# Kernel tuning notes

Hardware: AMD Instinct MI355X
Metric: run time of the kernel (lower is better)

## Reference

```python
import jax, jax.numpy as jnp
import numpy as np

UNITS = [100, 80, 50, 30]
D_IN = 64


def _lstm_layer(x, Wx, Wh, b):
    # x: [B, T, D]; Wx: [D, 4u]; Wh: [u, 4u]; b: [4u]
    B = x.shape[0]
    u = Wh.shape[0]
    # precompute input contribution for all timesteps: [B, T, 4u]
    xg = jnp.einsum('btd,dg->btg', x, Wx) + b

    def step(carry, xg_t):
        h, c = carry
        g = xg_t + h @ Wh                      # [B, 4u]
        i, f, cbar, o = jnp.split(g, 4, axis=-1)
        i = jax.nn.sigmoid(i)
        f = jax.nn.sigmoid(f)
        o = jax.nn.sigmoid(o)
        c = f * c + i * jnp.tanh(cbar)
        h = o * jnp.tanh(c)
        return (h, c), h

    init = (jnp.zeros((B, u), x.dtype), jnp.zeros((B, u), x.dtype))
    (h_final, _), hs = jax.lax.scan(step, init, jnp.swapaxes(xg, 0, 1))
    return jnp.swapaxes(hs, 0, 1), h_final  # [B, T, u], [B, u]


def setup_inputs() -> dict:
    key = jax.random.key(0)
    ks = jax.random.split(key, 16)
    B, T = 256, 1024
    inp = {"sequence": jax.random.normal(ks[0], (B, T, D_IN), dtype=jnp.float32)}
    d_in = D_IN
    for li, u in enumerate(UNITS):
        s_x = 1.0 / np.sqrt(d_in)
        s_h = 1.0 / np.sqrt(u)
        inp[f"Wx{li}"] = jax.random.normal(ks[1 + 3 * li], (d_in, 4 * u), dtype=jnp.float32) * s_x
        inp[f"Wh{li}"] = jax.random.normal(ks[2 + 3 * li], (u, 4 * u), dtype=jnp.float32) * s_h
        inp[f"b{li}"] = jnp.zeros((4 * u,), dtype=jnp.float32)
        d_in = u
    inp["W_out"] = jax.random.normal(ks[13], (UNITS[-1], 1), dtype=jnp.float32) / np.sqrt(UNITS[-1])
    inp["b_out"] = jnp.zeros((1,), dtype=jnp.float32)
    return inp


def reference(sequence, Wx0, Wh0, b0, Wx1, Wh1, b1, Wx2, Wh2, b2, Wx3, Wh3, b3, W_out, b_out):
    # 4 stacked LSTM layers; dropout is identity at inference.
    x, _ = _lstm_layer(sequence, Wx0, Wh0, b0)   # [B, T, 100]
    x, _ = _lstm_layer(x, Wx1, Wh1, b1)          # [B, T, 80]
    x, _ = _lstm_layer(x, Wx2, Wh2, b2)          # [B, T, 50]
    _, h = _lstm_layer(x, Wx3, Wh3, b3)          # final state [B, 30]
    return h @ W_out + b_out                     # [B, 1]
```

## Files before the change

### kernel.cpp

```cpp
#include <hip/hip_runtime.h>


#define BATCH 256
#define TSTEPS 1024

__device__ __forceinline__ float sigm(float x) {
    return 1.0f / (1.0f + __expf(-x));
}

__device__ __forceinline__ float tanh_fast(float x) {
    float ax = fabsf(x);
    float e = __expf(2.0f * ax);
    float r = 1.0f - 2.0f / (e + 1.0f);
    return copysignf(r, x);
}

template<int DIN, int U, int SPLIT, int S, int BLOCK, bool LAST>
__global__ __launch_bounds__(BLOCK, 1)
void lstm_layer(const float* __restrict__ xin,
                const float* __restrict__ Wx,
                const float* __restrict__ Wh,
                const float* __restrict__ bias,
                float* __restrict__ xout,
                const float* __restrict__ Wout,
                const float* __restrict__ bout,
                float* __restrict__ dout)
{
    constexpr int G  = 4 * U;
    constexpr int K  = DIN + U;
    constexpr int KP = SPLIT * S;
    static_assert(KP >= K, "slice coverage");
    static_assert((S % 4) == 0, "float4 alignment");

    const int b   = blockIdx.x;
    const int tid = threadIdx.x;
    const int u   = tid / SPLIT;
    const int s   = tid % SPLIT;
    const bool active = (u < U);
    const int uu  = active ? u : 0;

    __shared__ __align__(16) float s_xh[2][KP];

    for (int i = tid; i < 2 * KP; i += BLOCK) ((float*)s_xh)[i] = 0.0f;

    float w[4][S];
    float bj[4];
#pragma unroll
    for (int g = 0; g < 4; ++g) {
        const int col = g * U + uu;
        bj[g] = bias[col];
#pragma unroll
        for (int kk = 0; kk < S; ++kk) {
            const int k = s * S + kk;
            float v = 0.0f;
            if (k < DIN)    v = Wx[k * G + col];
            else if (k < K) v = Wh[(k - DIN) * G + col];
            w[g][kk] = v;
        }
    }

    const float* xrow = xin + (size_t)b * TSTEPS * DIN;
    if (tid < DIN) s_xh[0][tid] = xrow[tid];
    __syncthreads();

    float c = 0.0f;
    int cur = 0;

    for (int t = 0; t < TSTEPS; ++t, cur ^= 1) {
        float xn = 0.0f;
        if (t + 1 < TSTEPS && tid < DIN) xn = xrow[(size_t)(t + 1) * DIN + tid];

        float a0 = 0.0f, a1 = 0.0f, a2 = 0.0f, a3 = 0.0f;
        const float* xh = &s_xh[cur][s * S];
#pragma unroll
        for (int kk = 0; kk < S; kk += 4) {
            float4 v = *(const float4*)(xh + kk);
            a0 = fmaf(v.x, w[0][kk + 0], a0);
            a0 = fmaf(v.y, w[0][kk + 1], a0);
            a0 = fmaf(v.z, w[0][kk + 2], a0);
            a0 = fmaf(v.w, w[0][kk + 3], a0);
            a1 = fmaf(v.x, w[1][kk + 0], a1);
            a1 = fmaf(v.y, w[1][kk + 1], a1);
            a1 = fmaf(v.z, w[1][kk + 2], a1);
            a1 = fmaf(v.w, w[1][kk + 3], a1);
            a2 = fmaf(v.x, w[2][kk + 0], a2);
            a2 = fmaf(v.y, w[2][kk + 1], a2);
            a2 = fmaf(v.z, w[2][kk + 2], a2);
            a2 = fmaf(v.w, w[2][kk + 3], a2);
            a3 = fmaf(v.x, w[3][kk + 0], a3);
            a3 = fmaf(v.y, w[3][kk + 1], a3);
            a3 = fmaf(v.z, w[3][kk + 2], a3);
            a3 = fmaf(v.w, w[3][kk + 3], a3);
        }

#pragma unroll
        for (int d = SPLIT >> 1; d > 0; d >>= 1) {
            a0 += __shfl_down(a0, d);
            a1 += __shfl_down(a1, d);
            a2 += __shfl_down(a2, d);
            a3 += __shfl_down(a3, d);
        }

        const int nxt = cur ^ 1;
        if (active && s == 0) {
            const float fi = sigm(a0 + bj[0]);
            const float ff = sigm(a1 + bj[1]);
            const float tc = tanh_fast(a2 + bj[2]);
            const float fo = sigm(a3 + bj[3]);
            c = ff * c + fi * tc;
            const float h = fo * tanh_fast(c);
            s_xh[nxt][DIN + u] = h;
            if (!LAST) xout[((size_t)b * TSTEPS + t) * U + u] = h;
        }
        if (tid < DIN) s_xh[nxt][tid] = xn;
        __syncthreads();
    }

    if (LAST && tid == 0) {
        float acc = bout[0];
#pragma unroll
        for (int k = 0; k < U; ++k) acc = fmaf(s_xh[cur][DIN + k], Wout[k], acc);
        dout[b] = acc;
    }
}

extern "C" void kernel_launch(void* const* d_in, const int* in_sizes, int n_in,
                              void* d_out, int out_size, void* d_ws, size_t ws_size,
                              hipStream_t stream)
{
    const float* seq  = (const float*)d_in[0];
    const float* Wx0  = (const float*)d_in[1];
    const float* Wh0  = (const float*)d_in[2];
    const float* b0   = (const float*)d_in[3];
    const float* Wx1  = (const float*)d_in[4];
    const float* Wh1  = (const float*)d_in[5];
    const float* b1   = (const float*)d_in[6];
    const float* Wx2  = (const float*)d_in[7];
    const float* Wh2  = (const float*)d_in[8];
    const float* b2   = (const float*)d_in[9];
    const float* Wx3  = (const float*)d_in[10];
    const float* Wh3  = (const float*)d_in[11];
    const float* b3   = (const float*)d_in[12];
    const float* Wout = (const float*)d_in[13];
    const float* bout = (const float*)d_in[14];
    float* out = (float*)d_out;

    float* ws = (float*)d_ws;
    float* X1 = ws;
    float* X2 = ws + (size_t)BATCH * TSTEPS * 100;
    float* X3 = ws;

    dim3 grid(BATCH);

    lstm_layer<64, 100, 4, 44, 448, false><<<grid, 448, 0, stream>>>(
        seq, Wx0, Wh0, b0, X1, nullptr, nullptr, nullptr);
    lstm_layer<100, 80, 4, 48, 320, false><<<grid, 320, 0, stream>>>(
        X1, Wx1, Wh1, b1, X2, nullptr, nullptr, nullptr);
    lstm_layer<80, 50, 4, 36, 256, false><<<grid, 256, 0, stream>>>(
        X2, Wx2, Wh2, b2, X3, nullptr, nullptr, nullptr);
    lstm_layer<50, 30, 4, 20, 128, true><<<grid, 128, 0, stream>>>(
        X3, Wx3, Wh3, b3, nullptr, Wout, bout, out);
}
```

Baseline: 3.586 ms.

## Split K across 8 lanes with packed FMA and DPP reduction

Each hidden unit's dot product is now split across 8 threads instead of 4, so blocks are twice as large and each thread holds a shorter weight slice. The inner loop uses two-wide float vectors so the compiler can emit packed FMA instructions, and the cross-lane sum uses DPP row operations in place of shuffle-down. The aim is to shorten the serial per-timestep critical path of the recurrence. In exchange the block is larger, so the per-step barrier covers more waves, and the DPP reduction assumes each group of 8 lanes is aligned inside a row.

```diff
diff --git a/kernel.cpp b/kernel.cpp
--- a/kernel.cpp
+++ b/kernel.cpp
@@ -3,6 +3,29 @@
 
 #define BATCH 256
 #define TSTEPS 1024
+
+typedef float v2f __attribute__((ext_vector_type(2)));
+
+__device__ __forceinline__ v2f fma2(v2f a, v2f b, v2f c) {
+#if __has_builtin(__builtin_elementwise_fma)
+    return __builtin_elementwise_fma(a, b, c);
+#else
+    v2f r; r.x = fmaf(a.x, b.x, c.x); r.y = fmaf(a.y, b.y, c.y); return r;
+#endif
+}
+
+template<int CTRL>
+__device__ __forceinline__ float red_step(float v) {
+    int t = __builtin_amdgcn_update_dpp(0, __float_as_int(v), CTRL, 0xF, 0xF, true);
+    return v + __int_as_float(t);
+}
+
+__device__ __forceinline__ float red8(float v) {
+    v = red_step<0xB1>(v);
+    v = red_step<0x4E>(v);
+    v = red_step<0x141>(v);
+    return v;
+}
 
 __device__ __forceinline__ float sigm(float x) {
     return 1.0f / (1.0f + __expf(-x));
@@ -15,7 +38,7 @@
     return copysignf(r, x);
 }
 
-template<int DIN, int U, int SPLIT, int S, int BLOCK, bool LAST>
+template<int DIN, int U, int S, int BLOCK, bool LAST>
 __global__ __launch_bounds__(BLOCK, 1)
 void lstm_layer(const float* __restrict__ xin,
                 const float* __restrict__ Wx,
@@ -28,14 +51,14 @@
 {
     constexpr int G  = 4 * U;
     constexpr int K  = DIN + U;
-    constexpr int KP = SPLIT * S;
+    constexpr int KP = 8 * S;
     static_assert(KP >= K, "slice coverage");
     static_assert((S % 4) == 0, "float4 alignment");
 
     const int b   = blockIdx.x;
     const int tid = threadIdx.x;
-    const int u   = tid / SPLIT;
-    const int s   = tid % SPLIT;
+    const int u   = tid >> 3;
+    const int s   = tid & 7;
     const bool active = (u < U);
     const int uu  = active ? u : 0;
 
@@ -43,19 +66,24 @@
 
     for (int i = tid; i < 2 * KP; i += BLOCK) ((float*)s_xh)[i] = 0.0f;
 
-    float w[4][S];
+    v2f w2[4][S / 2];
     float bj[4];
 #pragma unroll
     for (int g = 0; g < 4; ++g) {
         const int col = g * U + uu;
         bj[g] = bias[col];
 #pragma unroll
-        for (int kk = 0; kk < S; ++kk) {
-            const int k = s * S + kk;
-            float v = 0.0f;
-            if (k < DIN)    v = Wx[k * G + col];
-            else if (k < K) v = Wh[(k - DIN) * G + col];
-            w[g][kk] = v;
+        for (int j = 0; j < S / 2; ++j) {
+            v2f v;
+#pragma unroll
+            for (int e = 0; e < 2; ++e) {
+                const int k = s * S + 2 * j + e;
+                float x = 0.0f;
+                if (k < DIN)    x = Wx[k * G + col];
+                else if (k < K) x = Wh[(k - DIN) * G + col];
+                v[e] = x;
+            }
+            w2[g][j] = v;
         }
     }
 
@@ -70,43 +98,35 @@
         float xn = 0.0f;
         if (t + 1 < TSTEPS && tid < DIN) xn = xrow[(size_t)(t + 1) * DIN + tid];
 
-        float a0 = 0.0f, a1 = 0.0f, a2 = 0.0f, a3 = 0.0f;
+        v2f a0 = {0.0f, 0.0f}, a1 = a0, a2 = a0, a3 = a0;
         const float* xh = &s_xh[cur][s * S];
 #pragma unroll
         for (int kk = 0; kk < S; kk += 4) {
             float4 v = *(const float4*)(xh + kk);
-            a0 = fmaf(v.x, w[0][kk + 0], a0);
-            a0 = fmaf(v.y, w[0][kk + 1], a0);
-            a0 = fmaf(v.z, w[0][kk + 2], a0);
-            a0 = fmaf(v.w, w[0][kk + 3], a0);
-            a1 = fmaf(v.x, w[1][kk + 0], a1);
-            a1 = fmaf(v.y, w[1][kk + 1], a1);
-            a1 = fmaf(v.z, w[1][kk + 2], a1);
-            a1 = fmaf(v.w, w[1][kk + 3], a1);
-            a2 = fmaf(v.x, w[2][kk + 0], a2);
-            a2 = fmaf(v.y, w[2][kk + 1], a2);
-            a2 = fmaf(v.z, w[2][kk + 2], a2);
-            a2 = fmaf(v.w, w[2][kk + 3], a2);
-            a3 = fmaf(v.x, w[3][kk + 0], a3);
-            a3 = fmaf(v.y, w[3][kk + 1], a3);
-            a3 = fmaf(v.z, w[3][kk + 2], a3);
-            a3 = fmaf(v.w, w[3][kk + 3], a3);
+            v2f lo = {v.x, v.y};
+            v2f hi = {v.z, v.w};
+            const int j = kk >> 1;
+            a0 = fma2(lo, w2[0][j], a0);
+            a0 = fma2(hi, w2[0][j + 1], a0);
+            a1 = fma2(lo, w2[1][j], a1);
+            a1 = fma2(hi, w2[1][j + 1], a1);
+            a2 = fma2(lo, w2[2][j], a2);
+            a2 = fma2(hi, w2[2][j + 1], a2);
+            a3 = fma2(lo, w2[3][j], a3);
+            a3 = fma2(hi, w2[3][j + 1], a3);
         }
 
-#pragma unroll
-        for (int d = SPLIT >> 1; d > 0; d >>= 1) {
-            a0 += __shfl_down(a0, d);
-            a1 += __shfl_down(a1, d);
-            a2 += __shfl_down(a2, d);
-            a3 += __shfl_down(a3, d);
-        }
+        float g0 = red8(a0.x + a0.y);
+        float g1 = red8(a1.x + a1.y);
+        float g2 = red8(a2.x + a2.y);
+        float g3 = red8(a3.x + a3.y);
 
         const int nxt = cur ^ 1;
         if (active && s == 0) {
-            const float fi = sigm(a0 + bj[0]);
-            const float ff = sigm(a1 + bj[1]);
-            const float tc = tanh_fast(a2 + bj[2]);
-            const float fo = sigm(a3 + bj[3]);
+            const float fi = sigm(g0 + bj[0]);
+            const float ff = sigm(g1 + bj[1]);
+            const float tc = tanh_fast(g2 + bj[2]);
+            const float fo = sigm(g3 + bj[3]);
             c = ff * c + fi * tc;
             const float h = fo * tanh_fast(c);
             s_xh[nxt][DIN + u] = h;
@@ -152,12 +172,12 @@
 
     dim3 grid(BATCH);
 
-    lstm_layer<64, 100, 4, 44, 448, false><<<grid, 448, 0, stream>>>(
+    lstm_layer<64, 100, 24, 832, false><<<grid, 832, 0, stream>>>(
         seq, Wx0, Wh0, b0, X1, nullptr, nullptr, nullptr);
-    lstm_layer<100, 80, 4, 48, 320, false><<<grid, 320, 0, stream>>>(
+    lstm_layer<100, 80, 24, 640, false><<<grid, 640, 0, stream>>>(
         X1, Wx1, Wh1, b1, X2, nullptr, nullptr, nullptr);
-    lstm_layer<80, 50, 4, 36, 256, false><<<grid, 256, 0, stream>>>(
+    lstm_layer<80, 50, 20, 448, false><<<grid, 448, 0, stream>>>(
         X2, Wx2, Wh2, b2, X3, nullptr, nullptr, nullptr);
-    lstm_layer<50, 30, 4, 20, 128, true><<<grid, 128, 0, stream>>>(
+    lstm_layer<50, 30, 12, 256, true><<<grid, 256, 0, stream>>>(
         X3, Wx3, Wh3, b3, nullptr, Wout, bout, out);
 }
```

New measurement: 3.763 ms. +4.9%, slower.
